# Kernel tuning notes

Hardware: AMD Instinct MI355X
Metric: run time of the kernel (lower is better)

## Reference

```python
import jax, jax.numpy as jnp
import numpy as np

TEMPERATURE = 1.0
SCALE = 0.1  # embedding scale so exp(-dist/T) stays in fp32 range


def setup_inputs() -> dict:
    key = jax.random.key(0)
    kt, ki, kg = jax.random.split(key, 3)
    B, D, G = 8192, 512, 16
    text_embeddings = jax.random.normal(kt, (B, D), dtype=jnp.float32) * SCALE
    image_embeddings = jax.random.normal(ki, (B, D), dtype=jnp.float32) * SCALE
    groups = jax.random.randint(kg, (B,), 0, G, dtype=jnp.int64)
    return {"text_embeddings": text_embeddings,
            "image_embeddings": image_embeddings,
            "groups": groups}


def _pairwise_l2(text, image):
    # ||t_i - m_j|| via squared-norm expansion; sqrt made grad-safe at 0
    sq = (jnp.sum(text * text, axis=1)[:, None]
          + jnp.sum(image * image, axis=1)[None, :]
          - 2.0 * text @ image.T)                      # [B, B]
    sq = jnp.maximum(sq, 0.0)
    safe = jnp.where(sq > 0, sq, 1.0)
    return jnp.where(sq > 0, jnp.sqrt(safe), 0.0)


def reference(text_embeddings, image_embeddings, groups):
    B = text_embeddings.shape[0]
    dist = _pairwise_l2(text_embeddings, image_embeddings)   # [B, B]
    sim = jnp.exp(-dist / TEMPERATURE)                       # [B, B]
    same = groups[:, None] == groups[None, :]                # [B, B] bool
    numerator = jnp.sum(jnp.where(same, sim, 0.0), axis=1)   # [B]
    denominator = jnp.sum(jnp.where(same, 0.0, sim), axis=1) # [B]
    valid = (numerator > 0) & (denominator > 0)
    ratio = jnp.where(valid, numerator / jnp.where(valid, denominator, 1.0), 1.0)
    loss_i = jnp.where(valid, -jnp.log(ratio), 0.0)
    return jnp.sum(loss_i) / B
```

## Files before the change

### kernel.cpp

```cpp
#include <hip/hip_runtime.h>
#include <hip/hip_bf16.h>
#include <stdint.h>

#define Bn 8192
#define Dk 512
#define SCALE1 0x7F7F7F7F

typedef __attribute__((ext_vector_type(8))) int   int8v;
typedef __attribute__((ext_vector_type(4))) int   int4v;
typedef __attribute__((ext_vector_type(16))) float f32x16;

__device__ __forceinline__ void gload_lds16(const uint8_t* g, const uint8_t* l) {
  __builtin_amdgcn_global_load_lds(
      (const __attribute__((address_space(1))) void*)g,
      (__attribute__((address_space(3))) void*)l,
      16, 0, 0);
}

__global__ __launch_bounds__(128) void prep_kernel(
    const float* __restrict__ T, const float* __restrict__ M,
    uint8_t* __restrict__ Tq, uint8_t* __restrict__ Mq,
    float* __restrict__ tn, float* __restrict__ mn)
{
  const int bid = blockIdx.x;
  const int row = bid & (Bn - 1);
  const bool isM = bid >= Bn;
  const float* __restrict__ src = isM ? M : T;
  unsigned* __restrict__ dst = (unsigned*)(isM ? Mq : Tq);
  const int tid = threadIdx.x;

  float4 v = reinterpret_cast<const float4*>(src + (size_t)row * Dk)[tid];
  float s = v.x * v.x + v.y * v.y + v.z * v.z + v.w * v.w;
  int p = __builtin_amdgcn_cvt_pk_fp8_f32(v.x, v.y, 0, false);
  p = __builtin_amdgcn_cvt_pk_fp8_f32(v.z, v.w, p, true);
  dst[(size_t)row * 128 + tid] = (unsigned)p;

  #pragma unroll
  for (int off = 32; off >= 1; off >>= 1) s += __shfl_xor(s, off, 64);
  __shared__ float ws2[2];
  if ((tid & 63) == 0) ws2[tid >> 6] = s;
  __syncthreads();
  if (tid == 0) (isM ? mn : tn)[row] = ws2[0] + ws2[1];
}

__global__ __launch_bounds__(512, 4) void gemm_epi_kernel(
    const uint8_t* __restrict__ Tq, const uint8_t* __restrict__ Mq,
    const float* __restrict__ tn, const float* __restrict__ mn,
    const int* __restrict__ groups,
    float2* __restrict__ part)
{
  extern __shared__ char smem[];
  uint8_t* As8 = (uint8_t*)smem;
  uint8_t* Bs8 = As8 + 3 * 16384;
  float2* tg_s = (float2*)(Bs8 + 3 * 8192);
  float2* mg_s = tg_s + 256;

  const int tid = threadIdx.x;
  const int wave = tid >> 6;
  const int lane = tid & 63;
  const int l31 = lane & 31, h = lane >> 5;

  const int bid = blockIdx.x;
  const int xcd = bid & 7, lidx = bid >> 3;
  const int by = xcd * 4 + (lidx & 3);
  const int bx = lidx >> 2;
  const int brow = by * 256;
  const int bcol = bx * 128;

  const int tc = wave & 3;
  const int ir = wave >> 2;

  if (tid < 256) {
    tg_s[tid] = make_float2(tn[brow + tid], __uint_as_float((unsigned)groups[brow + tid]));
  } else if (tid < 384) {
    const int t = tid - 256;
    mg_s[t] = make_float2(mn[bcol + t], __uint_as_float((unsigned)groups[bcol + t]));
  }

  int ldsT[2], ldsM;
  unsigned goffT[2], goffM;
  #pragma unroll
  for (int i = 0; i < 2; ++i) {
    const int c = i * 512 + tid;
    const int r = c >> 2;
    const int sc = (c & 3) ^ ((r >> 1) & 3);
    goffT[i] = (unsigned)(brow + r) * Dk + sc * 16;
    ldsT[i] = (i * 512 + wave * 64) * 16;
  }
  {
    const int c = tid;
    const int r = c >> 2;
    const int sc = (c & 3) ^ ((r >> 1) & 3);
    goffM = (unsigned)(bcol + r) * Dk + sc * 16;
    ldsM = wave * 64 * 16;
  }

  auto stage = [&](int t, int buf) {
    const int k0 = t * 64;
    gload_lds16(Tq + goffT[0] + k0, As8 + buf * 16384 + ldsT[0]);
    gload_lds16(Tq + goffT[1] + k0, As8 + buf * 16384 + ldsT[1]);
    gload_lds16(Mq + goffM + k0, Bs8 + buf * 8192 + ldsM);
  };

  int toffB[2], moffB[2];
  #pragma unroll
  for (int jt = 0; jt < 2; ++jt) {
    const int r = tc * 64 + jt * 32 + l31;
    toffB[jt] = r * 64 + (((h << 1) ^ ((r >> 1) & 3)) << 4);
  }
  #pragma unroll
  for (int it = 0; it < 2; ++it) {
    const int r = ir * 64 + it * 32 + l31;
    moffB[it] = r * 64 + (((h << 1) ^ ((r >> 1) & 3)) << 4);
  }

  f32x16 acc[2][2];
  #pragma unroll
  for (int it = 0; it < 2; ++it)
    #pragma unroll
    for (int jt = 0; jt < 2; ++jt)
      #pragma unroll
      for (int e = 0; e < 16; ++e)
        acc[it][jt][e] = 0.f;

  stage(0, 0); stage(1, 1);
  asm volatile("s_waitcnt vmcnt(3)" ::: "memory");
  __builtin_amdgcn_s_barrier();
  int kt = 0;

#define STEP(BUF, DO_STAGE, VMC)                                               \
  do {                                                                         \
    __builtin_amdgcn_s_barrier();                                              \
    if (DO_STAGE) stage(kt + 2, ((BUF) + 2) % 3);                              \
    asm volatile("s_waitcnt vmcnt(" #VMC ")" ::: "memory");                    \
    int8v tf[2], mf[2];                                                        \
    _Pragma("unroll")                                                          \
    for (int jt = 0; jt < 2; ++jt) {                                           \
      int4v lo = *(const int4v*)(As8 + (BUF) * 16384 + toffB[jt]);             \
      int4v hi = *(const int4v*)(As8 + (BUF) * 16384 + (toffB[jt] ^ 16));      \
      tf[jt] = __builtin_shufflevector(lo, hi, 0, 1, 2, 3, 4, 5, 6, 7);        \
    }                                                                          \
    _Pragma("unroll")                                                          \
    for (int it = 0; it < 2; ++it) {                                           \
      int4v lo = *(const int4v*)(Bs8 + (BUF) * 8192 + moffB[it]);              \
      int4v hi = *(const int4v*)(Bs8 + (BUF) * 8192 + (moffB[it] ^ 16));       \
      mf[it] = __builtin_shufflevector(lo, hi, 0, 1, 2, 3, 4, 5, 6, 7);        \
    }                                                                          \
    __builtin_amdgcn_s_setprio(1);                                             \
    _Pragma("unroll")                                                          \
    for (int it = 0; it < 2; ++it)                                             \
      _Pragma("unroll")                                                        \
      for (int jt = 0; jt < 2; ++jt)                                           \
        acc[it][jt] = __builtin_amdgcn_mfma_scale_f32_32x32x64_f8f6f4(         \
            mf[it], tf[jt], acc[it][jt], 0, 0, 0, SCALE1, 0, SCALE1);          \
    __builtin_amdgcn_s_setprio(0);                                             \
    ++kt;                                                                      \
  } while (0)

  STEP(0, true,  6);
  STEP(1, true,  6);
  STEP(2, true,  6);
  STEP(0, true,  6);
  STEP(1, true,  6);
  STEP(2, true,  6);
  STEP(0, false, 3);
  STEP(1, false, 0);
#undef STEP

  float2* red = reinterpret_cast<float2*>(As8);

  float nv[2] = {0.f, 0.f}, dv[2] = {0.f, 0.f};
  const int tlA = tc * 64 + l31;
  const int tlB = tlA + 32;
  const float2 tgA = tg_s[tlA];
  const float2 tgB = tg_s[tlB];
  #pragma unroll
  for (int it = 0; it < 2; ++it) {
    #pragma unroll
    for (int reg = 0; reg < 16; ++reg) {
      const int crow = (reg & 3) + 8 * (reg >> 2) + 4 * h;
      const float2 mg = mg_s[ir * 64 + it * 32 + crow];
      const unsigned gm = __float_as_uint(mg.y);
      {
        const float sq = fmaxf(tgA.x + mg.x - 2.0f * acc[it][0][reg], 0.f);
        const float sim = __builtin_amdgcn_exp2f(-1.4426950408889634f *
                                                 __builtin_amdgcn_sqrtf(sq));
        if (__float_as_uint(tgA.y) == gm) nv[0] += sim; else dv[0] += sim;
      }
      {
        const float sq = fmaxf(tgB.x + mg.x - 2.0f * acc[it][1][reg], 0.f);
        const float sim = __builtin_amdgcn_exp2f(-1.4426950408889634f *
                                                 __builtin_amdgcn_sqrtf(sq));
        if (__float_as_uint(tgB.y) == gm) nv[1] += sim; else dv[1] += sim;
      }
    }
  }
  __syncthreads();
  const int slot = ir * 2 + h;
  red[slot * 256 + tlA] = make_float2(nv[0], dv[0]);
  red[slot * 256 + tlB] = make_float2(nv[1], dv[1]);
  __syncthreads();
  if (tid < 256) {
    float n = 0.f, d = 0.f;
    #pragma unroll
    for (int s = 0; s < 4; ++s) {
      const float2 v = red[s * 256 + tid];
      n += v.x; d += v.y;
    }
    part[(size_t)bx * Bn + brow + tid] = make_float2(n, d);
  }
}

__global__ __launch_bounds__(256) void finalize1_kernel(
    const float2* __restrict__ part, float* __restrict__ bsum)
{
  const int i = blockIdx.x * 256 + threadIdx.x;
  float nv = 0.f, dv = 0.f;
  #pragma unroll 8
  for (int p = 0; p < 64; ++p) {
    const float2 v = part[(size_t)p * Bn + i];
    nv += v.x; dv += v.y;
  }
  float li = (nv > 0.f && dv > 0.f)
      ? (__builtin_amdgcn_logf(dv) - __builtin_amdgcn_logf(nv)) * 0.69314718055994531f
      : 0.f;
  #pragma unroll
  for (int off = 32; off >= 1; off >>= 1) li += __shfl_xor(li, off, 64);
  __shared__ float ws4[4];
  if ((threadIdx.x & 63) == 0) ws4[threadIdx.x >> 6] = li;
  __syncthreads();
  if (threadIdx.x == 0) bsum[blockIdx.x] = ws4[0] + ws4[1] + ws4[2] + ws4[3];
}

__global__ void finalize2_kernel(const float* __restrict__ bsum, float* __restrict__ out)
{
  float s = (threadIdx.x < 32) ? bsum[threadIdx.x] : 0.f;
  #pragma unroll
  for (int off = 32; off >= 1; off >>= 1) s += __shfl_xor(s, off, 64);
  if (threadIdx.x == 0) out[0] = s / (float)Bn;
}

extern "C" void kernel_launch(void* const* d_in, const int* in_sizes, int n_in,
                              void* d_out, int out_size, void* d_ws, size_t ws_size,
                              hipStream_t stream) {
  const float* T = (const float*)d_in[0];
  const float* M = (const float*)d_in[1];
  const int* groups = (const int*)d_in[2];

  char* ws = (char*)d_ws;
  uint8_t* Tq = (uint8_t*)ws;
  uint8_t* Mq = (uint8_t*)(ws + (size_t)Bn * Dk);
  float* tn  = (float*)(ws + (size_t)Bn * Dk * 2);
  float* mn  = tn + Bn;
  float2* part = (float2*)(mn + Bn);
  float* bsum = (float*)(part + (size_t)64 * Bn);

  const int smem_bytes = 3 * 16384 + 3 * 8192 + 256 * 8 + 128 * 8;
  hipFuncSetAttribute((const void*)gemm_epi_kernel,
                      hipFuncAttributeMaxDynamicSharedMemorySize, smem_bytes);

  prep_kernel<<<2 * Bn, 128, 0, stream>>>(T, M, Tq, Mq, tn, mn);
  gemm_epi_kernel<<<2048, 512, smem_bytes, stream>>>(Tq, Mq, tn, mn, groups, part);
  finalize1_kernel<<<Bn / 256, 256, 0, stream>>>(part, bsum);
  finalize2_kernel<<<1, 64, 0, stream>>>(bsum, (float*)d_out);
}
```

Before: 64.87 us.

## Pre-tile fp8 operands into panel-contiguous layout in prep kernel

The prep kernel now processes 32 rows per block and writes the fp8-quantized embeddings into a blocked layout. In that layout each GEMM block's per-k-step tile is one contiguous 16KB (T) or 8KB (M) chunk arranged in MFMA fragment order. The GEMM then streams fully contiguous global loads directly into LDS and reads fragments at simple offsets, with no XOR swizzle. This is meant to cut global-load address overhead and improve coalescing in the main GEMM, and to cut the prep kernel's launch count. The risk is LDS bank conflicts from the unswizzled fragment reads, plus more complex prep stores.

```diff
diff --git a/kernel.cpp b/kernel.cpp
--- a/kernel.cpp
+++ b/kernel.cpp
@@ -17,30 +17,69 @@
       16, 0, 0);
 }
 
-__global__ __launch_bounds__(128) void prep_kernel(
+__global__ __launch_bounds__(256) void prep_kernel(
     const float* __restrict__ T, const float* __restrict__ M,
     uint8_t* __restrict__ Tq, uint8_t* __restrict__ Mq,
     float* __restrict__ tn, float* __restrict__ mn)
 {
-  const int bid = blockIdx.x;
-  const int row = bid & (Bn - 1);
-  const bool isM = bid >= Bn;
+  __shared__ uint32_t lds[4096];
+  __shared__ float pn[8][33];
+
+  const int b = blockIdx.x;
+  const bool isM = b >= 256;
+  const int pb = b & 255;
+  const int rbase = pb * 32;
   const float* __restrict__ src = isM ? M : T;
-  unsigned* __restrict__ dst = (unsigned*)(isM ? Mq : Tq);
-  const int tid = threadIdx.x;
-
-  float4 v = reinterpret_cast<const float4*>(src + (size_t)row * Dk)[tid];
-  float s = v.x * v.x + v.y * v.y + v.z * v.z + v.w * v.w;
-  int p = __builtin_amdgcn_cvt_pk_fp8_f32(v.x, v.y, 0, false);
-  p = __builtin_amdgcn_cvt_pk_fp8_f32(v.z, v.w, p, true);
-  dst[(size_t)row * 128 + tid] = (unsigned)p;
-
-  #pragma unroll
-  for (int off = 32; off >= 1; off >>= 1) s += __shfl_xor(s, off, 64);
-  __shared__ float ws2[2];
-  if ((tid & 63) == 0) ws2[tid >> 6] = s;
-  __syncthreads();
-  if (tid == 0) (isM ? mn : tn)[row] = ws2[0] + ws2[1];
+  uint8_t* __restrict__ dstq = isM ? Mq : Tq;
+  float* __restrict__ nrm = isM ? mn : tn;
+
+  const int t = threadIdx.x;
+  const int c8 = t >> 5;
+  const int r = t & 31;
+
+  const float4* rowp = (const float4*)(src + (size_t)(rbase + r) * Dk) + c8 * 16;
+  float s = 0.f;
+  #pragma unroll
+  for (int sl = 0; sl < 4; ++sl) {
+    uint32_t d[4];
+    #pragma unroll
+    for (int j = 0; j < 4; ++j) {
+      const float4 v = rowp[sl * 4 + j];
+      s += v.x * v.x + v.y * v.y + v.z * v.z + v.w * v.w;
+      int p = __builtin_amdgcn_cvt_pk_fp8_f32(v.x, v.y, 0, false);
+      p = __builtin_amdgcn_cvt_pk_fp8_f32(v.z, v.w, p, true);
+      d[j] = (uint32_t)p;
+    }
+    #pragma unroll
+    for (int j = 0; j < 4; ++j)
+      lds[c8 * 512 + sl * 128 + r * 4 + j] = d[j];
+  }
+  pn[c8][r] = s;
+  __syncthreads();
+
+  if (t < 32) {
+    float a = 0.f;
+    #pragma unroll
+    for (int k = 0; k < 8; ++k) a += pn[k][t];
+    nrm[rbase + t] = a;
+  }
+
+  const int kt = t >> 5;
+  const int off = (t & 31) * 64;
+  uint8_t* dst;
+  if (!isM) {
+    const int by = rbase >> 8;
+    const int g = (rbase & 255) >> 5;
+    dst = dstq + (size_t)by * 131072 + (size_t)kt * 16384 + g * 2048 + off;
+  } else {
+    const int bx = rbase >> 7;
+    const int g = (rbase & 127) >> 5;
+    dst = dstq + (size_t)bx * 65536 + (size_t)kt * 8192 + g * 2048 + off;
+  }
+  const uint32_t* sp = lds + t * 16;
+  #pragma unroll
+  for (int j = 0; j < 4; ++j)
+    *(int4v*)(dst + j * 16) = *(const int4v*)(sp + j * 4);
 }
 
 __global__ __launch_bounds__(512, 4) void gemm_epi_kernel(
@@ -77,42 +116,31 @@
     mg_s[t] = make_float2(mn[bcol + t], __uint_as_float((unsigned)groups[bcol + t]));
   }
 
-  int ldsT[2], ldsM;
-  unsigned goffT[2], goffM;
+  const uint8_t* Tpan = Tq + (size_t)by * 131072;
+  const uint8_t* Mpan = Mq + (size_t)bx * 65536;
+  int ldsT[2];
+  unsigned goffT[2];
   #pragma unroll
   for (int i = 0; i < 2; ++i) {
-    const int c = i * 512 + tid;
-    const int r = c >> 2;
-    const int sc = (c & 3) ^ ((r >> 1) & 3);
-    goffT[i] = (unsigned)(brow + r) * Dk + sc * 16;
+    goffT[i] = (unsigned)(i * 512 + tid) * 16;
     ldsT[i] = (i * 512 + wave * 64) * 16;
   }
-  {
-    const int c = tid;
-    const int r = c >> 2;
-    const int sc = (c & 3) ^ ((r >> 1) & 3);
-    goffM = (unsigned)(bcol + r) * Dk + sc * 16;
-    ldsM = wave * 64 * 16;
-  }
+  const unsigned goffM = (unsigned)tid * 16;
+  const int ldsM = wave * 64 * 16;
 
   auto stage = [&](int t, int buf) {
-    const int k0 = t * 64;
-    gload_lds16(Tq + goffT[0] + k0, As8 + buf * 16384 + ldsT[0]);
-    gload_lds16(Tq + goffT[1] + k0, As8 + buf * 16384 + ldsT[1]);
-    gload_lds16(Mq + goffM + k0, Bs8 + buf * 8192 + ldsM);
+    gload_lds16(Tpan + (unsigned)t * 16384 + goffT[0], As8 + buf * 16384 + ldsT[0]);
+    gload_lds16(Tpan + (unsigned)t * 16384 + goffT[1], As8 + buf * 16384 + ldsT[1]);
+    gload_lds16(Mpan + (unsigned)t * 8192 + goffM, Bs8 + buf * 8192 + ldsM);
   };
 
   int toffB[2], moffB[2];
   #pragma unroll
-  for (int jt = 0; jt < 2; ++jt) {
-    const int r = tc * 64 + jt * 32 + l31;
-    toffB[jt] = r * 64 + (((h << 1) ^ ((r >> 1) & 3)) << 4);
-  }
-  #pragma unroll
-  for (int it = 0; it < 2; ++it) {
-    const int r = ir * 64 + it * 32 + l31;
-    moffB[it] = r * 64 + (((h << 1) ^ ((r >> 1) & 3)) << 4);
-  }
+  for (int jt = 0; jt < 2; ++jt)
+    toffB[jt] = (tc * 2 + jt) * 2048 + h * 1024 + l31 * 16;
+  #pragma unroll
+  for (int it = 0; it < 2; ++it)
+    moffB[it] = (ir * 2 + it) * 2048 + h * 1024 + l31 * 16;
 
   f32x16 acc[2][2];
   #pragma unroll
@@ -137,13 +165,13 @@
     _Pragma("unroll")                                                          \
     for (int jt = 0; jt < 2; ++jt) {                                           \
       int4v lo = *(const int4v*)(As8 + (BUF) * 16384 + toffB[jt]);             \
-      int4v hi = *(const int4v*)(As8 + (BUF) * 16384 + (toffB[jt] ^ 16));      \
+      int4v hi = *(const int4v*)(As8 + (BUF) * 16384 + toffB[jt] + 512);       \
       tf[jt] = __builtin_shufflevector(lo, hi, 0, 1, 2, 3, 4, 5, 6, 7);        \
     }                                                                          \
     _Pragma("unroll")                                                          \
     for (int it = 0; it < 2; ++it) {                                           \
       int4v lo = *(const int4v*)(Bs8 + (BUF) * 8192 + moffB[it]);              \
-      int4v hi = *(const int4v*)(Bs8 + (BUF) * 8192 + (moffB[it] ^ 16));       \
+      int4v hi = *(const int4v*)(Bs8 + (BUF) * 8192 + moffB[it] + 512);        \
       mf[it] = __builtin_shufflevector(lo, hi, 0, 1, 2, 3, 4, 5, 6, 7);        \
     }                                                                          \
     __builtin_amdgcn_s_setprio(1);                                             \
@@ -259,7 +287,7 @@
   hipFuncSetAttribute((const void*)gemm_epi_kernel,
                       hipFuncAttributeMaxDynamicSharedMemorySize, smem_bytes);
 
-  prep_kernel<<<2 * Bn, 128, 0, stream>>>(T, M, Tq, Mq, tn, mn);
+  prep_kernel<<<512, 256, 0, stream>>>(T, M, Tq, Mq, tn, mn);
   gemm_epi_kernel<<<2048, 512, smem_bytes, stream>>>(Tq, Mq, tn, mn, groups, part);
   finalize1_kernel<<<Bn / 256, 256, 0, stream>>>(part, bsum);
   finalize2_kernel<<<1, 64, 0, stream>>>(bsum, (float*)d_out);
```

Measured after the change: 61.83 us. 4.7% less time.
